# Kernel optimization log

Measured on AMD Instinct MI355X. Metric: run time of the kernel, lower is better.

The kernel has to match this reference:

```python
import jax, jax.numpy as jnp
import numpy as np

D_MODEL = 1024
NUM_HEADS = 16
D_K = D_MODEL // NUM_HEADS
B, S = 4, 2048


def setup_inputs() -> dict:
    key = jax.random.key(0)
    ks = jax.random.split(key, 11)
    scale = 1.0 / np.sqrt(D_MODEL)
    inp = {
        "query": jax.random.normal(ks[0], (B, S, D_MODEL), dtype=jnp.float32),
        "key": jax.random.normal(ks[1], (B, S, D_MODEL), dtype=jnp.float32),
        "value": jax.random.normal(ks[2], (B, S, D_MODEL), dtype=jnp.float32),
        "mask": jnp.tril(jnp.ones((S, S), dtype=jnp.int32))[None, None, :, :],
        "Wq": jax.random.normal(ks[3], (D_MODEL, D_MODEL), dtype=jnp.float32) * scale,
        "bq": jax.random.normal(ks[4], (D_MODEL,), dtype=jnp.float32) * scale,
        "Wk": jax.random.normal(ks[5], (D_MODEL, D_MODEL), dtype=jnp.float32) * scale,
        "bk": jax.random.normal(ks[6], (D_MODEL,), dtype=jnp.float32) * scale,
        "Wv": jax.random.normal(ks[7], (D_MODEL, D_MODEL), dtype=jnp.float32) * scale,
        "bv": jax.random.normal(ks[8], (D_MODEL,), dtype=jnp.float32) * scale,
        "Wo": jax.random.normal(ks[9], (D_MODEL, D_MODEL), dtype=jnp.float32) * scale,
        "bo": jax.random.normal(ks[10], (D_MODEL,), dtype=jnp.float32) * scale,
    }
    return inp


def reference(query, key, value, mask, Wq, bq, Wk, bk, Wv, bv, Wo, bo):
    b, s, _ = query.shape
    # Linear projections (torch Linear: x @ W.T + b), split into heads -> [B,H,S,Dk]
    Q = (query @ Wq.T + bq).reshape(b, s, NUM_HEADS, D_K).transpose(0, 2, 1, 3)
    K = (key @ Wk.T + bk).reshape(b, s, NUM_HEADS, D_K).transpose(0, 2, 1, 3)
    V = (value @ Wv.T + bv).reshape(b, s, NUM_HEADS, D_K).transpose(0, 2, 1, 3)
    scores = jnp.einsum("bhqd,bhkd->bhqk", Q, K) / jnp.sqrt(jnp.float32(D_K))
    scores = jnp.where(mask == 0, -jnp.inf, scores)
    attn = jax.nn.softmax(scores, axis=-1)  # dropout p=0.0 -> identity
    x = jnp.einsum("bhqk,bhkd->bhqd", attn, V)
    x = x.transpose(0, 2, 1, 3).reshape(b, s, D_MODEL)
    return x @ Wo.T + bo
```

## Files before the change

### kernel.cpp

```cpp
#include <hip/hip_runtime.h>
#include <cstdint>

#define DM   1024
#define NH   16
#define DKd  64
#define Bb   4
#define Ss   2048

using bf16x8_t = __attribute__((ext_vector_type(8))) __bf16;
using bf16x2_t = __attribute__((ext_vector_type(2))) __bf16;
using f32x4_t  = __attribute__((ext_vector_type(4))) float;
using u16x4_t  = __attribute__((ext_vector_type(4))) unsigned short;
using u16x8_t  = __attribute__((ext_vector_type(8))) unsigned short;
using u32x2_t  = __attribute__((ext_vector_type(2))) unsigned int;

#define MFMA16(a, b, c) __builtin_amdgcn_mfma_f32_16x16x32_bf16((a), (b), (c), 0, 0, 0)

__device__ __forceinline__ void mfma_k16(f32x4_t& c, u32x2_t a, u32x2_t b) {
  asm("v_mfma_f32_16x16x16_bf16 %0, %1, %2, %0" : "+v"(c) : "v"(a), "v"(b));
}

__device__ __forceinline__ unsigned short f2bf(float f) {
  union { float f; unsigned u; } v; v.f = f;
  unsigned r = v.u + 0x7fffu + ((v.u >> 16) & 1u);
  return (unsigned short)(r >> 16);
}

__device__ __forceinline__ void gl16(const void* g, void* l) {
  __builtin_amdgcn_global_load_lds(
      (const __attribute__((address_space(1))) void*)g,
      (__attribute__((address_space(3))) void*)l, 16, 0, 0);
}

struct CvtArgs {
  const float* src[4];
  unsigned short* dst[4];
  int n[4];
};

__global__ void cvt_kernel(CvtArgs a) {
  const int seg = blockIdx.y;
  const float* __restrict__ s = a.src[seg];
  unsigned short* __restrict__ d = a.dst[seg];
  const int n = a.n[seg];
  const int step = gridDim.x * blockDim.x * 4;
  for (int i = (blockIdx.x * blockDim.x + threadIdx.x) * 4; i < n; i += step) {
    f32x4_t v = *(const f32x4_t*)(s + i);
    u16x4_t r;
    r[0] = f2bf(v[0]); r[1] = f2bf(v[1]); r[2] = f2bf(v[2]); r[3] = f2bf(v[3]);
    *(u16x4_t*)(d + i) = r;
  }
}

struct GemmArgs {
  const unsigned short* A[3];
  const float* A32[3];
  const unsigned short* W[3];
  const float* bias[3];
  void* out[3];
  float scl[3];
  int epi[3];
};

__device__ __forceinline__ void gemm_epilogue(
    const GemmArgs& ga, int z, int epi, float scl, const float* bias,
    f32x4_t (&acc)[4][4], int m0, int n0, int wm, int wn, int qr, int kg) {
#pragma unroll
  for (int ni = 0; ni < 4; ++ni) {
    const int col = n0 + wn * 64 + ni * 16 + qr;
    const float bi = bias[col];
#pragma unroll
    for (int mi = 0; mi < 4; ++mi) {
      const int mb = m0 + wm * 64 + mi * 16 + kg * 4;
      float vv[4];
#pragma unroll
      for (int j = 0; j < 4; ++j) vv[j] = (acc[mi][ni][j] + bi) * scl;
      if (epi == 0) {
        unsigned short* O = (unsigned short*)ga.out[z];
#pragma unroll
        for (int j = 0; j < 4; ++j) {
          const int m = mb + j;
          O[(size_t)((m >> 11) * NH + (col >> 6)) * (Ss * DKd) +
            (size_t)(m & (Ss - 1)) * DKd + (col & 63)] = f2bf(vv[j]);
        }
      } else if (epi == 2) {
        unsigned short* O = (unsigned short*)ga.out[z];
        u16x4_t r;
#pragma unroll
        for (int j = 0; j < 4; ++j) r[j] = f2bf(vv[j]);
        const int b = mb >> 11, s = mb & (Ss - 1);
        *(u16x4_t*)&O[((size_t)(b * NH + (col >> 6)) * DKd + (col & 63)) * Ss + s] = r;
      } else {
        float* O = (float*)ga.out[z];
#pragma unroll
        for (int j = 0; j < 4; ++j) O[(size_t)(mb + j) * 1024 + col] = vv[j];
      }
    }
  }
}

__global__ __launch_bounds__(256, 4) void gemm_qkv(GemmArgs ga) {
  const int L = blockIdx.x + 8 * (blockIdx.y + 64 * blockIdx.z);
  const int xcd = L & 7;
  const int sidx = L >> 3;
  const int xw = sidx & 7;
  const int grp = sidx >> 3;
  const int z = grp >> 3;
  const int yw = (grp & 7) * 8 + xcd;

  const float* __restrict__ A32 = ga.A32[z];
  const unsigned short* __restrict__ W = ga.W[z];
  const float* __restrict__ bias = ga.bias[z];
  const float scl = ga.scl[z];
  const int epi = ga.epi[z];

  __shared__ __align__(16) float sA32[128 * 32];
  __shared__ __align__(16) unsigned short sB[128 * 32];

  const int tid  = threadIdx.x;
  const int lane = tid & 63;
  const int wid  = tid >> 6;
  const int wm   = wid >> 1, wn = wid & 1;
  const int m0 = yw * 128, n0 = xw * 128;
  const int qr = lane & 15, kg = lane >> 4;

  const int e0 = tid * 8;
  const int e1 = e0 + 2048;
  const int r0 = e0 >> 5, c0 = e0 & 31;
  const int r1 = e1 >> 5, c1 = e1 & 31;

  const int arow = tid >> 3;
  const int swzc = (tid & 7) ^ ((tid >> 3) & 7);

  f32x4_t acc[4][4];
#pragma unroll
  for (int mi = 0; mi < 4; ++mi)
#pragma unroll
    for (int ni = 0; ni < 4; ++ni) acc[mi][ni] = {0.f, 0.f, 0.f, 0.f};

  for (int kt = 0; kt < 32; ++kt) {
    const int k0 = kt * 32;
#pragma unroll
    for (int j = 0; j < 4; ++j)
      gl16(A32 + (size_t)(m0 + arow + j * 32) * 1024 + k0 + swzc * 4,
           &sA32[tid * 4 + j * 1024]);
    gl16(W + (size_t)(n0 + r0) * 1024 + k0 + c0, &sB[e0]);
    gl16(W + (size_t)(n0 + r1) * 1024 + k0 + c1, &sB[e1]);
    __syncthreads();

    bf16x8_t af[4], bfr[4];
    const int sw = qr & 7;
#pragma unroll
    for (int i = 0; i < 4; ++i) {
      const int row = wm * 64 + i * 16 + qr;
      const f32x4_t alo =
          *(const f32x4_t*)&sA32[row * 32 + (((2 * kg) ^ sw) << 2)];
      const f32x4_t ahi =
          *(const f32x4_t*)&sA32[row * 32 + (((2 * kg + 1) ^ sw) << 2)];
      u16x8_t aw;
#pragma unroll
      for (int j = 0; j < 4; ++j) {
        aw[j] = f2bf(alo[j]);
        aw[4 + j] = f2bf(ahi[j]);
      }
      af[i] = __builtin_bit_cast(bf16x8_t, aw);
      bfr[i] = *(const bf16x8_t*)&sB[(wn * 64 + i * 16 + qr) * 32 + kg * 8];
    }
    __builtin_amdgcn_s_setprio(1);
#pragma unroll
    for (int mi = 0; mi < 4; ++mi)
#pragma unroll
      for (int ni = 0; ni < 4; ++ni)
        acc[mi][ni] = MFMA16(af[mi], bfr[ni], acc[mi][ni]);
    __builtin_amdgcn_s_setprio(0);
    __syncthreads();
  }

  gemm_epilogue(ga, z, epi, scl, bias, acc, m0, n0, wm, wn, qr, kg);
}

__global__ __launch_bounds__(256, 4) void gemm_bt(GemmArgs ga) {
  const int L = blockIdx.x + 8 * (blockIdx.y + 64 * blockIdx.z);
  const int xcd = L & 7;
  const int sidx = L >> 3;
  const int xw = sidx & 7;
  const int grp = sidx >> 3;
  const int z = grp >> 3;
  const int yw = (grp & 7) * 8 + xcd;

  const unsigned short* __restrict__ A = ga.A[z];
  const unsigned short* __restrict__ W = ga.W[z];
  const float* __restrict__ bias = ga.bias[z];
  const float scl = ga.scl[z];
  const int epi = ga.epi[z];

  __shared__ __align__(16) unsigned short sA[128 * 32];
  __shared__ __align__(16) unsigned short sB[128 * 32];

  const int tid  = threadIdx.x;
  const int lane = tid & 63;
  const int wid  = tid >> 6;
  const int wm   = wid >> 1, wn = wid & 1;
  const int m0 = yw * 128, n0 = xw * 128;
  const int qr = lane & 15, kg = lane >> 4;

  const int e0 = tid * 8;
  const int e1 = e0 + 2048;
  const int r0 = e0 >> 5, c0 = e0 & 31;
  const int r1 = e1 >> 5, c1 = e1 & 31;

  f32x4_t acc[4][4];
#pragma unroll
  for (int mi = 0; mi < 4; ++mi)
#pragma unroll
    for (int ni = 0; ni < 4; ++ni) acc[mi][ni] = {0.f, 0.f, 0.f, 0.f};

  for (int kt = 0; kt < 32; ++kt) {
    const int k0 = kt * 32;
    gl16(A + (size_t)(m0 + r0) * 1024 + k0 + c0, &sA[e0]);
    gl16(A + (size_t)(m0 + r1) * 1024 + k0 + c1, &sA[e1]);
    gl16(W + (size_t)(n0 + r0) * 1024 + k0 + c0, &sB[e0]);
    gl16(W + (size_t)(n0 + r1) * 1024 + k0 + c1, &sB[e1]);
    __syncthreads();

    bf16x8_t af[4], bfr[4];
#pragma unroll
    for (int i = 0; i < 4; ++i) {
      af[i]  = *(const bf16x8_t*)&sA[(wm * 64 + i * 16 + qr) * 32 + kg * 8];
      bfr[i] = *(const bf16x8_t*)&sB[(wn * 64 + i * 16 + qr) * 32 + kg * 8];
    }
#pragma unroll
    for (int mi = 0; mi < 4; ++mi)
#pragma unroll
      for (int ni = 0; ni < 4; ++ni)
        acc[mi][ni] = MFMA16(af[mi], bfr[ni], acc[mi][ni]);
    __syncthreads();
  }

  gemm_epilogue(ga, z, epi, scl, bias, acc, m0, n0, wm, wn, qr, kg);
}

__global__ __launch_bounds__(256, 3) void attn_kernel(
    const unsigned short* __restrict__ Qp, const unsigned short* __restrict__ Kp,
    const unsigned short* __restrict__ Vt, unsigned short* __restrict__ X) {
  const int x = blockIdx.x, y = blockIdx.y;
  const int bh = x * 8 + (y & 7);
  const int pr = y >> 3;

  const int tid = threadIdx.x, lane = tid & 63, w = tid >> 6;
  const int qr = lane & 15, kg = lane >> 4;

  const unsigned short* Qb = Qp + (size_t)bh * Ss * DKd;
  const unsigned short* Kb = Kp + (size_t)bh * Ss * DKd;
  const unsigned short* Vb = Vt + (size_t)bh * Ss * DKd;

  __shared__ __align__(16) unsigned short kbuf[2][4096];
  __shared__ __align__(16) unsigned short vbuf[2][4096];

  const int R0 = tid >> 3, c80 = (tid & 7) ^ (R0 & 7);
  const int R1 = R0 + 32,  c81 = (tid & 7) ^ (R1 & 7);

  const int bq = bh >> 4, hh = bh & 15;

#pragma unroll
  for (int half = 0; half < 2; ++half) {
    const int jsub = half == 0 ? (15 - pr) : pr;
    const int qbase = jsub * 128;
    const int ntile = 2 * jsub + 2;
    const int qrowA = qbase + w * 32 + qr;
    const int qrowB = qrowA + 16;

    const bf16x8_t qfA0 = *(const bf16x8_t*)&Qb[(size_t)qrowA * DKd + kg * 8];
    const bf16x8_t qfA1 = *(const bf16x8_t*)&Qb[(size_t)qrowA * DKd + 32 + kg * 8];
    const bf16x8_t qfB0 = *(const bf16x8_t*)&Qb[(size_t)qrowB * DKd + kg * 8];
    const bf16x8_t qfB1 = *(const bf16x8_t*)&Qb[(size_t)qrowB * DKd + 32 + kg * 8];

    float lA = 0.f, lB = 0.f;
    f32x4_t o[2][4];
#pragma unroll
    for (int g = 0; g < 2; ++g)
#pragma unroll
      for (int nd = 0; nd < 4; ++nd) o[g][nd] = {0.f, 0.f, 0.f, 0.f};

    int cur = 0;
    gl16(Kb + (size_t)R0 * DKd + c80 * 8, &kbuf[0][tid * 8]);
    gl16(Kb + (size_t)R1 * DKd + c81 * 8, &kbuf[0][tid * 8 + 2048]);
    gl16(Vb + (size_t)R0 * Ss + c80 * 8, &vbuf[0][tid * 8]);
    gl16(Vb + (size_t)R1 * Ss + c81 * 8, &vbuf[0][tid * 8 + 2048]);
    __syncthreads();

    for (int t = 0; t < ntile; ++t) {
      if (t + 1 < ntile) {
        const int kv0 = (t + 1) * 64;
        const int nb = cur ^ 1;
        gl16(Kb + (size_t)(kv0 + R0) * DKd + c80 * 8, &kbuf[nb][tid * 8]);
        gl16(Kb + (size_t)(kv0 + R1) * DKd + c81 * 8, &kbuf[nb][tid * 8 + 2048]);
        gl16(Vb + (size_t)R0 * Ss + kv0 + c80 * 8, &vbuf[nb][tid * 8]);
        gl16(Vb + (size_t)R1 * Ss + kv0 + c81 * 8, &vbuf[nb][tid * 8 + 2048]);
      }

      const bool act = !(w < 2 && t == 2 * jsub + 1);
      if (act) {
        f32x4_t sA_[4], sB_[4];
#pragma unroll
        for (int ni = 0; ni < 4; ++ni) {
          sA_[ni] = {-8.f, -8.f, -8.f, -8.f};
          sB_[ni] = {-8.f, -8.f, -8.f, -8.f};
        }
        __builtin_amdgcn_s_setprio(1);
#pragma unroll
        for (int ni = 0; ni < 4; ++ni) {
          const int R = ni * 16 + qr;
          const bf16x8_t kf0 =
              *(const bf16x8_t*)&kbuf[cur][(R * 8 + (kg ^ (qr & 7))) * 8];
          const bf16x8_t kf1 =
              *(const bf16x8_t*)&kbuf[cur][(R * 8 + ((4 + kg) ^ (qr & 7))) * 8];
          sA_[ni] = MFMA16(kf0, qfA0, sA_[ni]);
          sA_[ni] = MFMA16(kf1, qfA1, sA_[ni]);
          sB_[ni] = MFMA16(kf0, qfB0, sB_[ni]);
          sB_[ni] = MFMA16(kf1, qfB1, sB_[ni]);
        }
        __builtin_amdgcn_s_setprio(0);

        if (t >= 2 * jsub) {
          const int off = (t == 2 * jsub) ? 0 : 64;
          const int rA = w * 32 + qr - off;
#pragma unroll
          for (int ni = 0; ni < 4; ++ni)
#pragma unroll
            for (int j = 0; j < 4; ++j) {
              const int c = ni * 16 + kg * 4 + j;
              if (c > rA) sA_[ni][j] = -1.0e30f;
              if (c > rA + 16) sB_[ni][j] = -1.0e30f;
            }
        }

        u32x2_t pbA[4], pbB[4];
#pragma unroll
        for (int ni = 0; ni < 4; ++ni) {
          float pa0 = exp2f(sA_[ni][0]), pa1 = exp2f(sA_[ni][1]);
          float pa2 = exp2f(sA_[ni][2]), pa3 = exp2f(sA_[ni][3]);
          lA += (pa0 + pa1) + (pa2 + pa3);
          bf16x2_t lo, hi;
          lo[0] = (__bf16)pa0; lo[1] = (__bf16)pa1;
          hi[0] = (__bf16)pa2; hi[1] = (__bf16)pa3;
          pbA[ni][0] = __builtin_bit_cast(unsigned, lo);
          pbA[ni][1] = __builtin_bit_cast(unsigned, hi);
          float pb0 = exp2f(sB_[ni][0]), pb1 = exp2f(sB_[ni][1]);
          float pb2 = exp2f(sB_[ni][2]), pb3 = exp2f(sB_[ni][3]);
          lB += (pb0 + pb1) + (pb2 + pb3);
          bf16x2_t lo2, hi2;
          lo2[0] = (__bf16)pb0; lo2[1] = (__bf16)pb1;
          hi2[0] = (__bf16)pb2; hi2[1] = (__bf16)pb3;
          pbB[ni][0] = __builtin_bit_cast(unsigned, lo2);
          pbB[ni][1] = __builtin_bit_cast(unsigned, hi2);
        }
        asm volatile("s_nop 1");

        __builtin_amdgcn_s_setprio(1);
#pragma unroll
        for (int nd = 0; nd < 4; ++nd) {
          const int rb = (qr + 16 * nd) * 64 + 4 * (kg & 1);
          const int ch = kg >> 1, sw = qr & 7;
          u32x2_t va0 = *(const u32x2_t*)&vbuf[cur][rb + 8 * ((ch + 0) ^ sw)];
          u32x2_t va1 = *(const u32x2_t*)&vbuf[cur][rb + 8 * ((ch + 2) ^ sw)];
          u32x2_t va2 = *(const u32x2_t*)&vbuf[cur][rb + 8 * ((ch + 4) ^ sw)];
          u32x2_t va3 = *(const u32x2_t*)&vbuf[cur][rb + 8 * ((ch + 6) ^ sw)];
          mfma_k16(o[0][nd], va0, pbA[0]);
          mfma_k16(o[0][nd], va1, pbA[1]);
          mfma_k16(o[0][nd], va2, pbA[2]);
          mfma_k16(o[0][nd], va3, pbA[3]);
          mfma_k16(o[1][nd], va0, pbB[0]);
          mfma_k16(o[1][nd], va1, pbB[1]);
          mfma_k16(o[1][nd], va2, pbB[2]);
          mfma_k16(o[1][nd], va3, pbB[3]);
        }
        __builtin_amdgcn_s_setprio(0);
      }

      __syncthreads();
      cur ^= 1;
    }

    float lsA = lA, lsB = lB;
    lsA += __shfl_xor(lsA, 16); lsA += __shfl_xor(lsA, 32);
    lsB += __shfl_xor(lsB, 16); lsB += __shfl_xor(lsB, 32);
    const float invA = 1.0f / lsA, invB = 1.0f / lsB;
#pragma unroll
    for (int nd = 0; nd < 4; ++nd) {
      u16x4_t rA, rB;
#pragma unroll
      for (int j = 0; j < 4; ++j) {
        rA[j] = f2bf(o[0][nd][j] * invA);
        rB[j] = f2bf(o[1][nd][j] * invB);
      }
      const int d = nd * 16 + kg * 4;
      *(u16x4_t*)&X[(size_t)(bq * Ss + qrowA) * DM + hh * DKd + d] = rA;
      *(u16x4_t*)&X[(size_t)(bq * Ss + qrowB) * DM + hh * DKd + d] = rB;
    }
  }
}

extern "C" void kernel_launch(void* const* d_in, const int* in_sizes, int n_in,
                              void* d_out, int out_size, void* d_ws, size_t ws_size,
                              hipStream_t stream) {
  const float* q  = (const float*)d_in[0];
  const float* k  = (const float*)d_in[1];
  const float* v  = (const float*)d_in[2];
  const float* Wq = (const float*)d_in[4];
  const float* bq = (const float*)d_in[5];
  const float* Wk = (const float*)d_in[6];
  const float* bk = (const float*)d_in[7];
  const float* Wv = (const float*)d_in[8];
  const float* bv = (const float*)d_in[9];
  const float* Wo = (const float*)d_in[10];
  const float* bo = (const float*)d_in[11];

  const size_t NIN = (size_t)Bb * Ss * DM;
  const size_t NW  = (size_t)DM * DM;

  unsigned short* ws  = (unsigned short*)d_ws;
  unsigned short* Wqb = ws;
  unsigned short* Wkb = Wqb + NW;
  unsigned short* Wvb = Wkb + NW;
  unsigned short* Wob = Wvb + NW;
  unsigned short* qb  = Wob + NW;
  unsigned short* Qp  = qb + NIN;
  unsigned short* Kp  = Qp + NIN;
  unsigned short* Vt  = Kp + NIN;
  unsigned short* X   = qb;

  CvtArgs ca{};
  ca.src[0] = Wq; ca.dst[0] = Wqb; ca.n[0] = (int)NW;
  ca.src[1] = Wk; ca.dst[1] = Wkb; ca.n[1] = (int)NW;
  ca.src[2] = Wv; ca.dst[2] = Wvb; ca.n[2] = (int)NW;
  ca.src[3] = Wo; ca.dst[3] = Wob; ca.n[3] = (int)NW;
  cvt_kernel<<<dim3(256, 4), 256, 0, stream>>>(ca);

  const float SC = 0.18033688011112042f;

  GemmArgs g1{};
  g1.A32[0] = q;   g1.A32[1] = k;   g1.A32[2] = v;
  g1.W[0] = Wqb;   g1.W[1] = Wkb;   g1.W[2] = Wvb;
  g1.bias[0] = bq; g1.bias[1] = bk; g1.bias[2] = bv;
  g1.out[0] = Qp;  g1.out[1] = Kp;  g1.out[2] = Vt;
  g1.scl[0] = SC;  g1.scl[1] = 1.f; g1.scl[2] = 1.f;
  g1.epi[0] = 0;   g1.epi[1] = 0;   g1.epi[2] = 2;
  gemm_qkv<<<dim3(8, 64, 3), 256, 0, stream>>>(g1);

  attn_kernel<<<dim3(8, 64), 256, 0, stream>>>(Qp, Kp, Vt, X);

  GemmArgs g2{};
  g2.A[0] = X; g2.W[0] = Wob; g2.bias[0] = bo; g2.out[0] = d_out;
  g2.scl[0] = 1.f; g2.epi[0] = 1;
  gemm_bt<<<dim3(8, 64, 1), 256, 0, stream>>>(g2);
}
```

Measured before the change: 191.5 us.

## Double-buffer LDS tiles in QKV and output projection GEMMs

Both projection GEMM kernels now keep two LDS buffers. The next K-tile's global-to-LDS loads are issued before the MFMA work on the current tile, so load latency can overlap with compute and one barrier per iteration goes away. The output GEMM also gains raised wave priority around its MFMA block. The cost is doubled LDS use per block, so the QKV kernel's launch-bounds occupancy hint drops from 4 to 3 blocks.

Measured after the change: 191.5 us. Within noise of the previous version (+0.0%).

```diff
diff --git a/kernel.cpp b/kernel.cpp
--- a/kernel.cpp
+++ b/kernel.cpp
@@ -99,7 +99,7 @@
   }
 }
 
-__global__ __launch_bounds__(256, 4) void gemm_qkv(GemmArgs ga) {
+__global__ __launch_bounds__(256, 3) void gemm_qkv(GemmArgs ga) {
   const int L = blockIdx.x + 8 * (blockIdx.y + 64 * blockIdx.z);
   const int xcd = L & 7;
   const int sidx = L >> 3;
@@ -114,8 +114,8 @@
   const float scl = ga.scl[z];
   const int epi = ga.epi[z];
 
-  __shared__ __align__(16) float sA32[128 * 32];
-  __shared__ __align__(16) unsigned short sB[128 * 32];
+  __shared__ __align__(16) float sA32[2][128 * 32];
+  __shared__ __align__(16) unsigned short sB[2][128 * 32];
 
   const int tid  = threadIdx.x;
   const int lane = tid & 63;
@@ -138,15 +138,22 @@
 #pragma unroll
     for (int ni = 0; ni < 4; ++ni) acc[mi][ni] = {0.f, 0.f, 0.f, 0.f};
 
+#define STAGE(b, kt)                                                        \
+  do {                                                                      \
+    const int k0_ = (kt) * 32;                                              \
+    _Pragma("unroll") for (int j = 0; j < 4; ++j)                           \
+        gl16(A32 + (size_t)(m0 + arow + j * 32) * 1024 + k0_ + swzc * 4,    \
+             &sA32[b][tid * 4 + j * 1024]);                                 \
+    gl16(W + (size_t)(n0 + r0) * 1024 + k0_ + c0, &sB[b][e0]);              \
+    gl16(W + (size_t)(n0 + r1) * 1024 + k0_ + c1, &sB[b][e1]);              \
+  } while (0)
+
+  STAGE(0, 0);
+  __syncthreads();
+
+  int cur = 0;
   for (int kt = 0; kt < 32; ++kt) {
-    const int k0 = kt * 32;
-#pragma unroll
-    for (int j = 0; j < 4; ++j)
-      gl16(A32 + (size_t)(m0 + arow + j * 32) * 1024 + k0 + swzc * 4,
-           &sA32[tid * 4 + j * 1024]);
-    gl16(W + (size_t)(n0 + r0) * 1024 + k0 + c0, &sB[e0]);
-    gl16(W + (size_t)(n0 + r1) * 1024 + k0 + c1, &sB[e1]);
-    __syncthreads();
+    if (kt + 1 < 32) STAGE(cur ^ 1, kt + 1);
 
     bf16x8_t af[4], bfr[4];
     const int sw = qr & 7;
@@ -154,9 +161,9 @@
     for (int i = 0; i < 4; ++i) {
       const int row = wm * 64 + i * 16 + qr;
       const f32x4_t alo =
-          *(const f32x4_t*)&sA32[row * 32 + (((2 * kg) ^ sw) << 2)];
+          *(const f32x4_t*)&sA32[cur][row * 32 + (((2 * kg) ^ sw) << 2)];
       const f32x4_t ahi =
-          *(const f32x4_t*)&sA32[row * 32 + (((2 * kg + 1) ^ sw) << 2)];
+          *(const f32x4_t*)&sA32[cur][row * 32 + (((2 * kg + 1) ^ sw) << 2)];
       u16x8_t aw;
 #pragma unroll
       for (int j = 0; j < 4; ++j) {
@@ -164,7 +171,7 @@
         aw[4 + j] = f2bf(ahi[j]);
       }
       af[i] = __builtin_bit_cast(bf16x8_t, aw);
-      bfr[i] = *(const bf16x8_t*)&sB[(wn * 64 + i * 16 + qr) * 32 + kg * 8];
+      bfr[i] = *(const bf16x8_t*)&sB[cur][(wn * 64 + i * 16 + qr) * 32 + kg * 8];
     }
     __builtin_amdgcn_s_setprio(1);
 #pragma unroll
@@ -173,8 +180,11 @@
       for (int ni = 0; ni < 4; ++ni)
         acc[mi][ni] = MFMA16(af[mi], bfr[ni], acc[mi][ni]);
     __builtin_amdgcn_s_setprio(0);
+
     __syncthreads();
+    cur ^= 1;
   }
+#undef STAGE
 
   gemm_epilogue(ga, z, epi, scl, bias, acc, m0, n0, wm, wn, qr, kg);
 }
@@ -194,8 +204,8 @@
   const float scl = ga.scl[z];
   const int epi = ga.epi[z];
 
-  __shared__ __align__(16) unsigned short sA[128 * 32];
-  __shared__ __align__(16) unsigned short sB[128 * 32];
+  __shared__ __align__(16) unsigned short sA[2][128 * 32];
+  __shared__ __align__(16) unsigned short sB[2][128 * 32];
 
   const int tid  = threadIdx.x;
   const int lane = tid & 63;
@@ -215,27 +225,40 @@
 #pragma unroll
     for (int ni = 0; ni < 4; ++ni) acc[mi][ni] = {0.f, 0.f, 0.f, 0.f};
 
+#define STAGE(b, kt)                                                     \
+  do {                                                                   \
+    const int k0_ = (kt) * 32;                                           \
+    gl16(A + (size_t)(m0 + r0) * 1024 + k0_ + c0, &sA[b][e0]);           \
+    gl16(A + (size_t)(m0 + r1) * 1024 + k0_ + c1, &sA[b][e1]);           \
+    gl16(W + (size_t)(n0 + r0) * 1024 + k0_ + c0, &sB[b][e0]);           \
+    gl16(W + (size_t)(n0 + r1) * 1024 + k0_ + c1, &sB[b][e1]);           \
+  } while (0)
+
+  STAGE(0, 0);
+  __syncthreads();
+
+  int cur = 0;
   for (int kt = 0; kt < 32; ++kt) {
-    const int k0 = kt * 32;
-    gl16(A + (size_t)(m0 + r0) * 1024 + k0 + c0, &sA[e0]);
-    gl16(A + (size_t)(m0 + r1) * 1024 + k0 + c1, &sA[e1]);
-    gl16(W + (size_t)(n0 + r0) * 1024 + k0 + c0, &sB[e0]);
-    gl16(W + (size_t)(n0 + r1) * 1024 + k0 + c1, &sB[e1]);
-    __syncthreads();
+    if (kt + 1 < 32) STAGE(cur ^ 1, kt + 1);
 
     bf16x8_t af[4], bfr[4];
 #pragma unroll
     for (int i = 0; i < 4; ++i) {
-      af[i]  = *(const bf16x8_t*)&sA[(wm * 64 + i * 16 + qr) * 32 + kg * 8];
-      bfr[i] = *(const bf16x8_t*)&sB[(wn * 64 + i * 16 + qr) * 32 + kg * 8];
+      af[i]  = *(const bf16x8_t*)&sA[cur][(wm * 64 + i * 16 + qr) * 32 + kg * 8];
+      bfr[i] = *(const bf16x8_t*)&sB[cur][(wn * 64 + i * 16 + qr) * 32 + kg * 8];
     }
+    __builtin_amdgcn_s_setprio(1);
 #pragma unroll
     for (int mi = 0; mi < 4; ++mi)
 #pragma unroll
       for (int ni = 0; ni < 4; ++ni)
         acc[mi][ni] = MFMA16(af[mi], bfr[ni], acc[mi][ni]);
+    __builtin_amdgcn_s_setprio(0);
+
     __syncthreads();
+    cur ^= 1;
   }
+#undef STAGE
 
   gemm_epilogue(ga, z, epi, scl, bias, acc, m0, n0, wm, wn, qr, kg);
 }
```
